# Kernel optimization log

Measured on AMD Instinct MI355X. Metric: run time of the kernel, lower is better.

## Reference

```python
import jax, jax.numpy as jnp
import numpy as np

N = 50000      # nodes
E = 800000     # edges
IN = 128       # in_channels
HID = 32       # hidden_channels per head
HEADS = 4
OUT = 16       # out_channels
NEG_SLOPE_ATT = 0.2   # GATv2Conv default negative_slope
NEG_SLOPE_ACT = 0.01  # F.leaky_relu default
EPS = 1e-16


def setup_inputs() -> dict:
    key = jax.random.key(0)
    ks = jax.random.split(key, 13)
    d1 = HEADS * HID  # 128
    g = lambda k, shape, fan: jax.random.normal(k, shape, jnp.float32) * (1.0 / np.sqrt(fan))
    return {
        "x": jax.random.normal(ks[0], (N, IN), jnp.float32),
        "edge_index": jax.random.randint(ks[1], (2, E), 0, N, dtype=jnp.int32),
        "edge_weight": jax.random.uniform(ks[2], (E,), jnp.float32),
        # conv1 (GATv2): lin_l, lin_r, att, bias
        "Wl1": g(ks[3], (IN, d1), IN), "Wr1": g(ks[4], (IN, d1), IN),
        "att1": g(ks[5], (HEADS, HID), HID), "b1": jnp.zeros((d1,), jnp.float32),
        # conv2
        "Wl2": g(ks[6], (d1, d1), d1), "Wr2": g(ks[7], (d1, d1), d1),
        "att2": g(ks[8], (HEADS, HID), HID), "b2": jnp.zeros((d1,), jnp.float32),
        # classifier
        "Wc": g(ks[9], (d1, OUT), d1), "bc": jnp.zeros((OUT,), jnp.float32),
    }


def gatv2_layer(x, Wl, Wr, att, bias, src, dst):
    n = x.shape[0]
    xl = (x @ Wl).reshape(n, HEADS, HID)  # source transform
    xr = (x @ Wr).reshape(n, HEADS, HID)  # target transform
    m = xl[src] + xr[dst]                                    # [Etot, H, C]
    e = jnp.sum(jax.nn.leaky_relu(m, NEG_SLOPE_ATT) * att, axis=-1)  # [Etot, H]
    # segment softmax over incoming edges of each target node
    emax = jax.ops.segment_max(e, dst, num_segments=n)       # [N, H]
    ex = jnp.exp(e - emax[dst])
    denom = jax.ops.segment_sum(ex, dst, num_segments=n)     # [N, H]
    alpha = ex / (denom[dst] + EPS)                          # [Etot, H]
    out = jax.ops.segment_sum(xl[src] * alpha[:, :, None], dst, num_segments=n)  # [N, H, C]
    return out.reshape(n, HEADS * HID) + bias


def reference(x, edge_index, edge_weight, Wl1, Wr1, att1, b1, Wl2, Wr2, att2, b2, Wc, bc):
    # GATv2Conv default add_self_loops=True
    loops = jnp.arange(N, dtype=edge_index.dtype)
    src = jnp.concatenate([edge_index[0], loops])
    dst = jnp.concatenate([edge_index[1], loops])
    h = gatv2_layer(x, Wl1, Wr1, att1, b1, src, dst)
    h = jax.nn.leaky_relu(h, NEG_SLOPE_ACT)
    h = gatv2_layer(h, Wl2, Wr2, att2, b2, src, dst)
    h = jax.nn.leaky_relu(h, NEG_SLOPE_ACT)
    logits = h @ Wc + bc
    return (logits, h)
```

## Files before the change

### kernel.cpp

```cpp
#include <hip/hip_runtime.h>
#include <hip/hip_fp16.h>


#define LOG2E 1.4426950408889634f

typedef short bf16x8 __attribute__((ext_vector_type(8)));
typedef float f32x4 __attribute__((ext_vector_type(4)));

__device__ __forceinline__ unsigned short f2bf(float f) {
  union { float f; unsigned u; } x; x.f = f;
  unsigned r = x.u + 0x7fffu + ((x.u >> 16) & 1u);
  return (unsigned short)(r >> 16);
}
__device__ __forceinline__ float bf2f(unsigned short h) {
  union { unsigned u; float f; } x; x.u = ((unsigned)h) << 16;
  return x.f;
}
__device__ __forceinline__ void split4(float4 v, ushort4& h, ushort4& l) {
  h.x = f2bf(v.x); l.x = f2bf(v.x - bf2f(h.x));
  h.y = f2bf(v.y); l.y = f2bf(v.y - bf2f(h.y));
  h.z = f2bf(v.z); l.z = f2bf(v.z - bf2f(h.z));
  h.w = f2bf(v.w); l.w = f2bf(v.w - bf2f(h.w));
}


__global__ __launch_bounds__(256) void zero_i32(int* __restrict__ p, int n) {
  int i = blockIdx.x * 256 + threadIdx.x;
  if (i < n) p[i] = 0;
}

__global__ __launch_bounds__(256) void count_kernel(const int* __restrict__ dst,
                                                    int* __restrict__ cnt, int E) {
  int i = blockIdx.x * 256 + threadIdx.x;
  if (i < E) atomicAdd(&cnt[dst[i]], 1);
}

__global__ __launch_bounds__(256) void scan_blk(const int* __restrict__ cnt,
                                                int* __restrict__ excl,
                                                int* __restrict__ bsum, int n) {
  __shared__ int s[256];
  int t = threadIdx.x, i = blockIdx.x * 256 + t;
  int v = (i < n) ? (cnt[i] + 1) : 0;
  s[t] = v;
  __syncthreads();
#pragma unroll
  for (int off = 1; off < 256; off <<= 1) {
    int u = (t >= off) ? s[t - off] : 0;
    __syncthreads();
    s[t] += u;
    __syncthreads();
  }
  if (i < n) excl[i] = s[t] - v;
  if (t == 255) bsum[blockIdx.x] = s[255];
}

__global__ __launch_bounds__(256) void scan_bsum(int* __restrict__ bsum, int nb,
                                                 int* __restrict__ row_start, int n) {
  __shared__ int s[256];
  int t = threadIdx.x;
  int v = (t < nb) ? bsum[t] : 0;
  s[t] = v;
  __syncthreads();
#pragma unroll
  for (int off = 1; off < 256; off <<= 1) {
    int u = (t >= off) ? s[t - off] : 0;
    __syncthreads();
    s[t] += u;
    __syncthreads();
  }
  if (t < nb) bsum[t] = s[t] - v;
  if (t == 255) row_start[n] = s[255];
}

__global__ __launch_bounds__(256) void scan_add(int* __restrict__ row_start,
                                                const int* __restrict__ bsum,
                                                int* __restrict__ wpos,
                                                int* __restrict__ csr, int n) {
  int i = blockIdx.x * 256 + threadIdx.x;
  if (i < n) {
    int r = row_start[i] + bsum[blockIdx.x];
    row_start[i] = r;
    wpos[i] = r + 1;
    csr[r] = i;
  }
}

__global__ __launch_bounds__(256) void scatter_kernel(const int* __restrict__ src,
                                                      const int* __restrict__ dst,
                                                      int* __restrict__ wpos,
                                                      int* __restrict__ csr,
                                                      int E, int sliceSize) {
  int slice = blockIdx.x & 7;
  int chunk = blockIdx.x >> 3;
  int nchunk = gridDim.x >> 3;
  int lo = slice * sliceSize, hi = lo + sliceSize;
  int per = (E + nchunk - 1) / nchunk;
  int b = chunk * per;
  int e = min(b + per, E);
  for (int i = b + threadIdx.x; i < e; i += 256) {
    int d = dst[i];
    if (d >= lo && d < hi) {
      int p = atomicAdd(&wpos[d], 1);
      csr[p] = src[i];
    }
  }
}

__global__ __launch_bounds__(256) void convert_W(const float* __restrict__ Wl1,
                                                 const float* __restrict__ Wr1,
                                                 const float* __restrict__ Wl2,
                                                 const float* __restrict__ Wr2,
                                                 unsigned short* __restrict__ BT1h,
                                                 unsigned short* __restrict__ BT1l,
                                                 unsigned short* __restrict__ BT2h,
                                                 unsigned short* __restrict__ BT2l) {
  int b = blockIdx.x;
  const float* Wl = (b < 128) ? Wl1 : Wl2;
  const float* Wr = (b < 128) ? Wr1 : Wr2;
  unsigned short* BTh = (b < 128) ? BT1h : BT2h;
  unsigned short* BTl = (b < 128) ? BT1l : BT2l;
  int idx = (b & 127) * 256 + threadIdx.x;
  int col = idx >> 7, k = idx & 127;
  float v = (col < 128) ? Wl[k * 128 + col] : Wr[k * 128 + (col - 128)];
  unsigned short h = f2bf(v);
  BTh[idx] = h;
  BTl[idx] = f2bf(v - bf2f(h));
}

template <bool FP32IN>
__global__ __launch_bounds__(256) void gemm_mfma(
    const float* __restrict__ Af,
    const unsigned short* __restrict__ Ah, const unsigned short* __restrict__ Al,
    const unsigned short* __restrict__ BTh, const unsigned short* __restrict__ BTl,
    __half* __restrict__ Cl, __half* __restrict__ Cr, int nrows) {
  __shared__ unsigned short sAh[128 * 32], sAl[128 * 32];
  __shared__ unsigned short sBh[64 * 32], sBl[64 * 32];
  int tid = threadIdx.x;
  int wave = tid >> 6, lane = tid & 63;
  int rowBase = blockIdx.x * 128;
  int colBase = blockIdx.y * 64;
  int rowHalf = (wave >> 1) * 64;
  int colHalf = (wave & 1) * 32;
  int l15 = lane & 15, quad = lane >> 4;

  f32x4 acc[4][2];
#pragma unroll
  for (int m = 0; m < 4; ++m)
#pragma unroll
    for (int n = 0; n < 2; ++n) acc[m][n] = (f32x4){0.f, 0.f, 0.f, 0.f};

  for (int kc = 0; kc < 4; ++kc) {
#pragma unroll
    for (int i = 0; i < 2; ++i) {
      int idx = tid + i * 256;
      int row = idx >> 2, seg = idx & 3;
      int gr = rowBase + row;
      if (FP32IN) {
        float4 v0 = make_float4(0.f, 0.f, 0.f, 0.f), v1 = v0;
        if (gr < nrows) {
          v0 = *(const float4*)&Af[(size_t)gr * 128 + kc * 32 + seg * 8];
          v1 = *(const float4*)&Af[(size_t)gr * 128 + kc * 32 + seg * 8 + 4];
        }
        ushort4 h0, l0, h1, l1;
        split4(v0, h0, l0);
        split4(v1, h1, l1);
        *(ushort4*)&sAh[row * 32 + seg * 8] = h0;
        *(ushort4*)&sAh[row * 32 + seg * 8 + 4] = h1;
        *(ushort4*)&sAl[row * 32 + seg * 8] = l0;
        *(ushort4*)&sAl[row * 32 + seg * 8 + 4] = l1;
      } else {
        uint4 vh = make_uint4(0, 0, 0, 0), vl = make_uint4(0, 0, 0, 0);
        if (gr < nrows) {
          vh = *(const uint4*)&Ah[(size_t)gr * 128 + kc * 32 + seg * 8];
          vl = *(const uint4*)&Al[(size_t)gr * 128 + kc * 32 + seg * 8];
        }
        *(uint4*)&sAh[row * 32 + seg * 8] = vh;
        *(uint4*)&sAl[row * 32 + seg * 8] = vl;
      }
    }
    {
      int col = tid >> 2, seg = tid & 3;
      *(uint4*)&sBh[col * 32 + seg * 8] =
          *(const uint4*)&BTh[(size_t)(colBase + col) * 128 + kc * 32 + seg * 8];
      *(uint4*)&sBl[col * 32 + seg * 8] =
          *(const uint4*)&BTl[(size_t)(colBase + col) * 128 + kc * 32 + seg * 8];
    }
    __syncthreads();

    bf16x8 afh[4], afl[4], bfh[2], bfl[2];
#pragma unroll
    for (int m = 0; m < 4; ++m) {
      int r = rowHalf + m * 16 + l15;
      afh[m] = *(const bf16x8*)&sAh[r * 32 + quad * 8];
      afl[m] = *(const bf16x8*)&sAl[r * 32 + quad * 8];
    }
#pragma unroll
    for (int n = 0; n < 2; ++n) {
      int cc = colHalf + n * 16 + l15;
      bfh[n] = *(const bf16x8*)&sBh[cc * 32 + quad * 8];
      bfl[n] = *(const bf16x8*)&sBl[cc * 32 + quad * 8];
    }
#pragma unroll
    for (int m = 0; m < 4; ++m)
#pragma unroll
      for (int n = 0; n < 2; ++n) {
        acc[m][n] = __builtin_amdgcn_mfma_f32_16x16x32_bf16(afh[m], bfh[n], acc[m][n], 0, 0, 0);
        acc[m][n] = __builtin_amdgcn_mfma_f32_16x16x32_bf16(afh[m], bfl[n], acc[m][n], 0, 0, 0);
        acc[m][n] = __builtin_amdgcn_mfma_f32_16x16x32_bf16(afl[m], bfh[n], acc[m][n], 0, 0, 0);
      }
    __syncthreads();
  }

  bool isL = (colBase < 128);
  __half* __restrict__ C = isL ? Cl : Cr;
  int cb = (isL ? colBase : colBase - 128) + colHalf;
#pragma unroll
  for (int m = 0; m < 4; ++m)
#pragma unroll
    for (int r = 0; r < 4; ++r) {
      int grow = rowBase + rowHalf + m * 16 + quad * 4 + r;
      if (grow < nrows) {
#pragma unroll
        for (int n = 0; n < 2; ++n)
          C[(size_t)grow * 128 + cb + n * 16 + l15] = __float2half(acc[m][n][r]);
      }
    }
}

__global__ __launch_bounds__(256) void gat_attn(const __half* __restrict__ xl,
                                                const __half* __restrict__ xr,
                                                const int* __restrict__ row_start,
                                                const int* __restrict__ csr,
                                                const float* __restrict__ att,
                                                const float* __restrict__ bias,
                                                float* __restrict__ ofp,
                                                unsigned short* __restrict__ oh_hi,
                                                unsigned short* __restrict__ oh_lo,
                                                int n_nodes) {
  int node = blockIdx.x * 4 + (threadIdx.x >> 6);
  if (node >= n_nodes) return;
  int lane = threadIdx.x & 63;
  int slot = lane >> 4;
  int l15 = lane & 15;
  int c0 = l15 * 8;

  float fxr[8];
  {
    uint4 raw = *(const uint4*)&xr[(size_t)node * 128 + c0];
    const __half* hp = (const __half*)&raw;
#pragma unroll
    for (int k = 0; k < 8; ++k) fxr[k] = __half2float(hp[k]);
  }
  float a06[8], a04[8];
  {
    float4 a0 = *(const float4*)&att[c0];
    float4 a1 = *(const float4*)&att[c0 + 4];
    float av[8] = {a0.x, a0.y, a0.z, a0.w, a1.x, a1.y, a1.z, a1.w};
    const float C06 = 0.6f * LOG2E, C04 = 0.4f * LOG2E;
#pragma unroll
    for (int k = 0; k < 8; ++k) { a06[k] = av[k] * C06; a04[k] = av[k] * C04; }
  }

  float acc[8];
#pragma unroll
  for (int k = 0; k < 8; ++k) acc[k] = 0.f;
  float lsum = 0.f;

#define EDGE_BODY(SRC, PVALID)                                                 \
  {                                                                            \
    uint4 raw = *(const uint4*)&xl[(size_t)(unsigned)(SRC)*128 + c0];          \
    const __half* hp = (const __half*)&raw;                                    \
    float e = 0.f;                                                             \
    _Pragma("unroll") for (int k = 0; k < 8; ++k) {                            \
      float t = __half2float(hp[k]) + fxr[k];                                  \
      e = fmaf(a06[k], t, e);                                                  \
      e = fmaf(a04[k], fabsf(t), e);                                           \
    }                                                                          \
    e += __shfl_xor(e, 1);                                                     \
    e += __shfl_xor(e, 2);                                                     \
    float p = (PVALID) ? __builtin_amdgcn_exp2f(e) : 0.f;                      \
    lsum += p;                                                                 \
    _Pragma("unroll") for (int k = 0; k < 8; ++k)                              \
        acc[k] = fmaf(p, __half2float(hp[k]), acc[k]);                         \
  }

  int beg = row_start[node], end = row_start[node + 1];
  int deg = end - beg;
  int fullEnd = beg + (deg & ~15);

  for (int base = beg; base < fullEnd; base += 16) {
    int b0 = base + 4 * slot;
    int s0 = csr[b0], s1 = csr[b0 + 1], s2 = csr[b0 + 2], s3 = csr[b0 + 3];
    EDGE_BODY(s0, true);
    EDGE_BODY(s1, true);
    EDGE_BODY(s2, true);
    EDGE_BODY(s3, true);
  }
  for (int base = fullEnd; base < end; base += 4) {
    int idx = base + slot;
    int src = csr[idx];
    EDGE_BODY(src, idx < end);
  }
#undef EDGE_BODY

  lsum += __shfl_xor(lsum, 16);
  lsum += __shfl_xor(lsum, 32);
#pragma unroll
  for (int k = 0; k < 8; ++k) {
    acc[k] += __shfl_xor(acc[k], 16);
    acc[k] += __shfl_xor(acc[k], 32);
  }

  if (slot == 0) {
    float4 b0v = *(const float4*)&bias[c0];
    float4 b1v = *(const float4*)&bias[c0 + 4];
    float bv[8] = {b0v.x, b0v.y, b0v.z, b0v.w, b1v.x, b1v.y, b1v.z, b1v.w};
    float inv = 1.f / (lsum + 1e-16f);
    float o[8];
#pragma unroll
    for (int k = 0; k < 8; ++k) {
      float v = fmaf(acc[k], inv, bv[k]);
      o[k] = fmaf(0.495f, fabsf(v), 0.505f * v);
    }
    if (ofp) {
      *(float4*)&ofp[(size_t)node * 128 + c0] = make_float4(o[0], o[1], o[2], o[3]);
      *(float4*)&ofp[(size_t)node * 128 + c0 + 4] = make_float4(o[4], o[5], o[6], o[7]);
    }
    if (oh_hi) {
      ushort4 h0, l0, h1, l1;
      split4(make_float4(o[0], o[1], o[2], o[3]), h0, l0);
      split4(make_float4(o[4], o[5], o[6], o[7]), h1, l1);
      *(ushort4*)&oh_hi[(size_t)node * 128 + c0] = h0;
      *(ushort4*)&oh_hi[(size_t)node * 128 + c0 + 4] = h1;
      *(ushort4*)&oh_lo[(size_t)node * 128 + c0] = l0;
      *(ushort4*)&oh_lo[(size_t)node * 128 + c0 + 4] = l1;
    }
  }
}

__global__ __launch_bounds__(256) void classifier_kernel(const float4* __restrict__ h4,
                                                         const float* __restrict__ Wc,
                                                         const float* __restrict__ bc,
                                                         float* __restrict__ logits,
                                                         int n) {
  __shared__ float sW[2048];
  __shared__ float sb[16];
  int t = threadIdx.x;
#pragma unroll
  for (int i = 0; i < 8; ++i) sW[t + i * 256] = Wc[t + i * 256];
  if (t < 16) sb[t] = bc[t];
  __syncthreads();
  int node = blockIdx.x * 256 + t;
  if (node >= n) return;
  float acc[16];
#pragma unroll
  for (int o = 0; o < 16; ++o) acc[o] = sb[o];
  for (int c4 = 0; c4 < 32; ++c4) {
    float4 hv = h4[(unsigned)node * 32 + c4];
    const float* w = &sW[c4 * 64];
#pragma unroll
    for (int o = 0; o < 16; ++o) {
      acc[o] = fmaf(hv.x, w[o], acc[o]);
      acc[o] = fmaf(hv.y, w[16 + o], acc[o]);
      acc[o] = fmaf(hv.z, w[32 + o], acc[o]);
      acc[o] = fmaf(hv.w, w[48 + o], acc[o]);
    }
  }
#pragma unroll
  for (int q = 0; q < 4; ++q)
    *(float4*)&logits[(size_t)node * 16 + q * 4] =
        make_float4(acc[q * 4], acc[q * 4 + 1], acc[q * 4 + 2], acc[q * 4 + 3]);
}


extern "C" void kernel_launch(void* const* d_in, const int* in_sizes, int n_in,
                              void* d_out, int out_size, void* d_ws, size_t ws_size,
                              hipStream_t stream) {
  const float* x    = (const float*)d_in[0];
  const int*   ei   = (const int*)d_in[1];
  const float* Wl1  = (const float*)d_in[3];
  const float* Wr1  = (const float*)d_in[4];
  const float* att1 = (const float*)d_in[5];
  const float* b1   = (const float*)d_in[6];
  const float* Wl2  = (const float*)d_in[7];
  const float* Wr2  = (const float*)d_in[8];
  const float* att2 = (const float*)d_in[9];
  const float* b2   = (const float*)d_in[10];
  const float* Wc   = (const float*)d_in[11];
  const float* bc   = (const float*)d_in[12];

  const int N = in_sizes[0] / 128;
  const int E = in_sizes[1] / 2;

  float* outp   = (float*)d_out;
  float* logits = outp;
  float* hout   = outp + (size_t)N * 16;
  unsigned short* regionA = (unsigned short*)hout;
  unsigned short* regionB = regionA + (size_t)N * 128;

  char* ws = (char*)d_ws;
  __half* xlbuf = (__half*)ws;                ws += (size_t)N * 128 * 2;
  __half* xrbuf = (__half*)ws;                ws += (size_t)N * 128 * 2;
  unsigned short* WT1h = (unsigned short*)ws; ws += 256 * 128 * 2;
  unsigned short* WT1l = (unsigned short*)ws; ws += 256 * 128 * 2;
  unsigned short* WT2h = (unsigned short*)ws; ws += 256 * 128 * 2;
  unsigned short* WT2l = (unsigned short*)ws; ws += 256 * 128 * 2;
  int* cnt       = (int*)ws;                  ws += (size_t)N * 4;
  int* row_start = (int*)ws;                  ws += (size_t)(N + 1) * 4;
  int* wpos      = (int*)ws;                  ws += (size_t)N * 4;
  int* bsum      = (int*)ws;                  ws += 256 * 4;
  int* csr       = (int*)ws;                  ws += (size_t)(E + N + 16) * 4;

  const int* esrc = ei;
  const int* edst = ei + E;

  int gN = (N + 255) / 256, gE = (E + 255) / 256;
  dim3 gGemm((N + 127) / 128, 4);
  int gAttn = (N + 3) / 4;
  int sliceSize = (N + 7) / 8;

  zero_i32<<<gN, 256, 0, stream>>>(cnt, N);
  count_kernel<<<gE, 256, 0, stream>>>(edst, cnt, E);
  scan_blk<<<gN, 256, 0, stream>>>(cnt, row_start, bsum, N);
  scan_bsum<<<1, 256, 0, stream>>>(bsum, gN, row_start, N);
  scan_add<<<gN, 256, 0, stream>>>(row_start, bsum, wpos, csr, N);
  scatter_kernel<<<1024, 256, 0, stream>>>(esrc, edst, wpos, csr, E, sliceSize);
  zero_i32<<<1, 256, 0, stream>>>(csr + E + N, 16);

  convert_W<<<256, 256, 0, stream>>>(Wl1, Wr1, Wl2, Wr2, WT1h, WT1l, WT2h, WT2l);

  gemm_mfma<true><<<gGemm, 256, 0, stream>>>(x, nullptr, nullptr, WT1h, WT1l,
                                             xlbuf, xrbuf, N);
  gat_attn<<<gAttn, 256, 0, stream>>>(xlbuf, xrbuf, row_start, csr, att1, b1,
                                      nullptr, regionA, regionB, N);

  gemm_mfma<false><<<gGemm, 256, 0, stream>>>(nullptr, regionA, regionB, WT2h, WT2l,
                                              xlbuf, xrbuf, N);
  gat_attn<<<gAttn, 256, 0, stream>>>(xlbuf, xrbuf, row_start, csr, att2, b2,
                                      hout, nullptr, nullptr, N);

  classifier_kernel<<<(N + 255) / 256, 256, 0, stream>>>((const float4*)hout, Wc, bc,
                                                         logits, N);
}
```

Before: 335.7 us.

## Pad GEMM LDS rows, slice count atomics by dst range, fold csr padding zeroing

Pads the shared-memory row stride in the MFMA GEMM from 32 to 40 elements to reduce LDS bank conflicts on the fragment reads. The degree-count kernel now uses the same 8-way dst-range slicing as the scatter kernel, so atomics from one block stay within a narrower address range. The separate tiny zeroing launch for the csr tail padding is folded into scan_add, saving one kernel launch. The count kernel now reads the dst array eight times over, trading extra reads for better atomic locality.

```diff
diff --git a/kernel.cpp b/kernel.cpp
--- a/kernel.cpp
+++ b/kernel.cpp
@@ -3,6 +3,7 @@
 
 
 #define LOG2E 1.4426950408889634f
+#define AST 40
 
 typedef short bf16x8 __attribute__((ext_vector_type(8)));
 typedef float f32x4 __attribute__((ext_vector_type(4)));
@@ -30,9 +31,19 @@
 }
 
 __global__ __launch_bounds__(256) void count_kernel(const int* __restrict__ dst,
-                                                    int* __restrict__ cnt, int E) {
-  int i = blockIdx.x * 256 + threadIdx.x;
-  if (i < E) atomicAdd(&cnt[dst[i]], 1);
+                                                    int* __restrict__ cnt,
+                                                    int E, int sliceSize) {
+  int slice = blockIdx.x & 7;
+  int chunk = blockIdx.x >> 3;
+  int nchunk = gridDim.x >> 3;
+  int lo = slice * sliceSize, hi = lo + sliceSize;
+  int per = (E + nchunk - 1) / nchunk;
+  int b = chunk * per;
+  int e = min(b + per, E);
+  for (int i = b + threadIdx.x; i < e; i += 256) {
+    int d = dst[i];
+    if (d >= lo && d < hi) atomicAdd(&cnt[d], 1);
+  }
 }
 
 __global__ __launch_bounds__(256) void scan_blk(const int* __restrict__ cnt,
@@ -75,7 +86,8 @@
 __global__ __launch_bounds__(256) void scan_add(int* __restrict__ row_start,
                                                 const int* __restrict__ bsum,
                                                 int* __restrict__ wpos,
-                                                int* __restrict__ csr, int n) {
+                                                int* __restrict__ csr,
+                                                int n, int padBase) {
   int i = blockIdx.x * 256 + threadIdx.x;
   if (i < n) {
     int r = row_start[i] + bsum[blockIdx.x];
@@ -83,6 +95,7 @@
     wpos[i] = r + 1;
     csr[r] = i;
   }
+  if (blockIdx.x == 0 && threadIdx.x < 16) csr[padBase + threadIdx.x] = 0;
 }
 
 __global__ __launch_bounds__(256) void scatter_kernel(const int* __restrict__ src,
@@ -133,8 +146,8 @@
     const unsigned short* __restrict__ Ah, const unsigned short* __restrict__ Al,
     const unsigned short* __restrict__ BTh, const unsigned short* __restrict__ BTl,
     __half* __restrict__ Cl, __half* __restrict__ Cr, int nrows) {
-  __shared__ unsigned short sAh[128 * 32], sAl[128 * 32];
-  __shared__ unsigned short sBh[64 * 32], sBl[64 * 32];
+  __shared__ unsigned short sAh[128 * AST], sAl[128 * AST];
+  __shared__ unsigned short sBh[64 * AST], sBl[64 * AST];
   int tid = threadIdx.x;
   int wave = tid >> 6, lane = tid & 63;
   int rowBase = blockIdx.x * 128;
@@ -164,25 +177,25 @@
         ushort4 h0, l0, h1, l1;
         split4(v0, h0, l0);
         split4(v1, h1, l1);
-        *(ushort4*)&sAh[row * 32 + seg * 8] = h0;
-        *(ushort4*)&sAh[row * 32 + seg * 8 + 4] = h1;
-        *(ushort4*)&sAl[row * 32 + seg * 8] = l0;
-        *(ushort4*)&sAl[row * 32 + seg * 8 + 4] = l1;
+        *(ushort4*)&sAh[row * AST + seg * 8] = h0;
+        *(ushort4*)&sAh[row * AST + seg * 8 + 4] = h1;
+        *(ushort4*)&sAl[row * AST + seg * 8] = l0;
+        *(ushort4*)&sAl[row * AST + seg * 8 + 4] = l1;
       } else {
         uint4 vh = make_uint4(0, 0, 0, 0), vl = make_uint4(0, 0, 0, 0);
         if (gr < nrows) {
           vh = *(const uint4*)&Ah[(size_t)gr * 128 + kc * 32 + seg * 8];
           vl = *(const uint4*)&Al[(size_t)gr * 128 + kc * 32 + seg * 8];
         }
-        *(uint4*)&sAh[row * 32 + seg * 8] = vh;
-        *(uint4*)&sAl[row * 32 + seg * 8] = vl;
+        *(uint4*)&sAh[row * AST + seg * 8] = vh;
+        *(uint4*)&sAl[row * AST + seg * 8] = vl;
       }
     }
     {
       int col = tid >> 2, seg = tid & 3;
-      *(uint4*)&sBh[col * 32 + seg * 8] =
+      *(uint4*)&sBh[col * AST + seg * 8] =
           *(const uint4*)&BTh[(size_t)(colBase + col) * 128 + kc * 32 + seg * 8];
-      *(uint4*)&sBl[col * 32 + seg * 8] =
+      *(uint4*)&sBl[col * AST + seg * 8] =
           *(const uint4*)&BTl[(size_t)(colBase + col) * 128 + kc * 32 + seg * 8];
     }
     __syncthreads();
@@ -191,14 +204,14 @@
 #pragma unroll
     for (int m = 0; m < 4; ++m) {
       int r = rowHalf + m * 16 + l15;
-      afh[m] = *(const bf16x8*)&sAh[r * 32 + quad * 8];
-      afl[m] = *(const bf16x8*)&sAl[r * 32 + quad * 8];
+      afh[m] = *(const bf16x8*)&sAh[r * AST + quad * 8];
+      afl[m] = *(const bf16x8*)&sAl[r * AST + quad * 8];
     }
 #pragma unroll
     for (int n = 0; n < 2; ++n) {
       int cc = colHalf + n * 16 + l15;
-      bfh[n] = *(const bf16x8*)&sBh[cc * 32 + quad * 8];
-      bfl[n] = *(const bf16x8*)&sBl[cc * 32 + quad * 8];
+      bfh[n] = *(const bf16x8*)&sBh[cc * AST + quad * 8];
+      bfl[n] = *(const bf16x8*)&sBl[cc * AST + quad * 8];
     }
 #pragma unroll
     for (int m = 0; m < 4; ++m)
@@ -414,18 +427,17 @@
   const int* esrc = ei;
   const int* edst = ei + E;
 
-  int gN = (N + 255) / 256, gE = (E + 255) / 256;
+  int gN = (N + 255) / 256;
   dim3 gGemm((N + 127) / 128, 4);
   int gAttn = (N + 3) / 4;
   int sliceSize = (N + 7) / 8;
 
   zero_i32<<<gN, 256, 0, stream>>>(cnt, N);
-  count_kernel<<<gE, 256, 0, stream>>>(edst, cnt, E);
+  count_kernel<<<1024, 256, 0, stream>>>(edst, cnt, E, sliceSize);
   scan_blk<<<gN, 256, 0, stream>>>(cnt, row_start, bsum, N);
   scan_bsum<<<1, 256, 0, stream>>>(bsum, gN, row_start, N);
-  scan_add<<<gN, 256, 0, stream>>>(row_start, bsum, wpos, csr, N);
+  scan_add<<<gN, 256, 0, stream>>>(row_start, bsum, wpos, csr, N, E + N);
   scatter_kernel<<<1024, 256, 0, stream>>>(esrc, edst, wpos, csr, E, sliceSize);
-  zero_i32<<<1, 256, 0, stream>>>(csr + E + N, 16);
 
   convert_W<<<256, 256, 0, stream>>>(Wl1, Wr1, Wl2, Wr2, WT1h, WT1l, WT2h, WT2l);
 
```

New measurement: 336.9 us. Within noise of the previous version (+0.4%).
